# Kernel optimization log

Hardware: AMD Instinct MI355X
Metric: run time of the kernel (lower is better)

## Reference

```python
import math
import jax, jax.numpy as jnp
import numpy as np

L, H, D, T_BLOCK, V = 4, 8, 512, 2048, 32000
B, T = 2, 2048
HD = D // H
EPS = 1e-5


def setup_inputs() -> dict:
    key = jax.random.key(0)
    ks = jax.random.split(key, 8)
    nrm = lambda k, s: (jax.random.normal(k, s, jnp.float32) * 0.02)
    return {
        "wte": nrm(ks[0], (V, D)),
        "wpe": nrm(ks[1], (T_BLOCK, D)),
        "ln1_w": jnp.ones((L, D), jnp.float32),
        "ln1_b": jnp.zeros((L, D), jnp.float32),
        "attn_w": nrm(ks[2], (L, D, 3 * D)),
        "attn_b": jnp.zeros((L, 3 * D), jnp.float32),
        "proj_w": nrm(ks[3], (L, D, D)),
        "proj_b": jnp.zeros((L, D), jnp.float32),
        "ln2_w": jnp.ones((L, D), jnp.float32),
        "ln2_b": jnp.zeros((L, D), jnp.float32),
        "fc_w": nrm(ks[4], (L, D, 4 * D)),
        "fc_b": jnp.zeros((L, 4 * D), jnp.float32),
        "fc2_w": nrm(ks[5], (L, 4 * D, D)),
        "fc2_b": jnp.zeros((L, D), jnp.float32),
        "lnf_w": jnp.ones((D,), jnp.float32),
        "lnf_b": jnp.zeros((D,), jnp.float32),
        "idx": jax.random.randint(ks[6], (B, T), 0, V, dtype=jnp.int32),
    }


def _layer_norm(x, w, b):
    mu = jnp.mean(x, axis=-1, keepdims=True)
    var = jnp.mean(jnp.square(x - mu), axis=-1, keepdims=True)
    return (x - mu) * jax.lax.rsqrt(var + EPS) * w + b


def _gpt_forward(wte, wpe, ln1_w, ln1_b, attn_w, attn_b, proj_w, proj_b,
                 ln2_w, ln2_b, fc_w, fc_b, fc2_w, fc2_b, lnf_w, lnf_b, idx):
    t = idx.shape[1]
    x = wte[idx] + wpe[:t]  # [B,T,D]
    causal = jnp.tril(jnp.ones((t, t), bool))  # [T,T]
    scale = 1.0 / math.sqrt(HD)

    def block(x, p):
        l1w, l1b, aw, ab, pw, pb, l2w, l2b, fw, fb, f2w, f2b = p
        h = _layer_norm(x, l1w, l1b)
        qkv = h @ aw + ab  # [B,T,3D]
        q, k, v = jnp.split(qkv, 3, axis=-1)
        q = q.reshape(B, t, H, HD).transpose(0, 2, 1, 3)  # [B,H,T,hd]
        k = k.reshape(B, t, H, HD).transpose(0, 2, 1, 3)
        v = v.reshape(B, t, H, HD).transpose(0, 2, 1, 3)
        att = jnp.einsum('bhqd,bhkd->bhqk', q, k) * scale
        att = jnp.where(causal, att, -jnp.inf)
        att = jax.nn.softmax(att, axis=-1)
        y = jnp.einsum('bhqk,bhkd->bhqd', att, v)
        y = y.transpose(0, 2, 1, 3).reshape(B, t, D)
        x = x + (y @ pw + pb)
        h2 = _layer_norm(x, l2w, l2b)
        x = x + (jax.nn.gelu(h2 @ fw + fb, approximate=False) @ f2w + f2b)
        return x, None

    x, _ = jax.lax.scan(block, x, (ln1_w, ln1_b, attn_w, attn_b, proj_w, proj_b,
                                   ln2_w, ln2_b, fc_w, fc_b, fc2_w, fc2_b))
    x = _layer_norm(x, lnf_w, lnf_b)
    return x @ wte.T  # tied lm_head: [B,T,V]


def reference(wte, wpe, ln1_w, ln1_b, attn_w, attn_b, proj_w, proj_b,
              ln2_w, ln2_b, fc_w, fc_b, fc2_w, fc2_b, lnf_w, lnf_b, idx):
    return _gpt_forward(wte, wpe, ln1_w, ln1_b, attn_w, attn_b, proj_w, proj_b,
                        ln2_w, ln2_b, fc_w, fc_b, fc2_w, fc2_b, lnf_w, lnf_b, idx)
```

## Files before the change

### kernel.cpp

```cpp
#include <hip/hip_runtime.h>
#include <math.h>

#define Lc 4
#define Hc 8
#define Dc 512
#define Vc 32000
#define Bc 2
#define Tc 2048
#define HDc 64
#define Mc (Bc*Tc)
#define D3c (3*Dc)
#define D4c (4*Dc)

typedef unsigned short u16;
typedef unsigned int u32;
typedef __attribute__((ext_vector_type(8))) short bf16x8;
typedef __attribute__((ext_vector_type(4))) float f32x4;

__device__ __forceinline__ float bf2f(u16 u){ union{u32 i; float f;} v; v.i=((u32)u)<<16; return v.f; }
__device__ __forceinline__ u16 f2bf(float f){ union{float f; u32 i;} v; v.f=f; u32 x=v.i; return (u16)((x + 0x7fffu + ((x>>16)&1u))>>16); }

__device__ __forceinline__ void gld16(const void* g, void* l){
    __builtin_amdgcn_global_load_lds((const __attribute__((address_space(1))) u32*)g,
                                     (__attribute__((address_space(3))) u32*)l, 16, 0, 0);
}

#define CVT_TOTAL 30043136
__device__ __attribute__((aligned(16))) u16  g_cvt[CVT_TOTAL];
__device__ __attribute__((aligned(16))) float g_x[(size_t)Mc*Dc];
__device__ __attribute__((aligned(16))) u16  g_h[(size_t)Mc*Dc];
__device__ u32 g_flag;

__global__ void detect_kernel(const u32* __restrict__ p){
    if(threadIdx.x == 0) g_flag = (p[0] == 0x3F800000u) ? 1u : 0u;
}

__global__ void convert_kernel(const void* __restrict__ src, u16* __restrict__ dst, int n){
    int i = blockIdx.x*256 + threadIdx.x;
    if(i >= n) return;
    if(g_flag) dst[i] = f2bf(((const float*)src)[i]);
    else       dst[i] = ((const u16*)src)[i];
}

__global__ void embed_kernel(const u16* __restrict__ wte, const u16* __restrict__ wpe,
                             const int* __restrict__ idx, float* __restrict__ x){
    int tid = blockIdx.x*256 + threadIdx.x;
    int row = tid >> 6;
    int d8 = (tid & 63) << 3;
    int tok = idx[row];
    int t = row & (Tc-1);
    union{uint4 v; u16 u[8];} a, b;
    a.v = *(const uint4*)(wte + (size_t)tok*Dc + d8);
    b.v = *(const uint4*)(wpe + (size_t)t*Dc + d8);
    float* o = x + (size_t)row*Dc + d8;
    #pragma unroll
    for(int i=0;i<8;i++) o[i] = bf2f(a.u[i]) + bf2f(b.u[i]);
}

__global__ void ln_kernel(const float* __restrict__ x, const u16* __restrict__ w,
                          const u16* __restrict__ b, u16* __restrict__ out){
    int wv = threadIdx.x >> 6, lane = threadIdx.x & 63;
    int row = blockIdx.x*4 + wv;
    const float* xr = x + (size_t)row*Dc + lane*8;
    float f[8];
    *(float4*)(f)   = *(const float4*)xr;
    *(float4*)(f+4) = *(const float4*)(xr+4);
    float s=0.f, s2=0.f;
    #pragma unroll
    for(int i=0;i<8;i++){ s+=f[i]; s2+=f[i]*f[i]; }
    #pragma unroll
    for(int off=32; off; off>>=1){ s += __shfl_xor(s,off,64); s2 += __shfl_xor(s2,off,64); }
    float mean = s*(1.f/Dc);
    float var  = s2*(1.f/Dc) - mean*mean;
    float rstd = rsqrtf(var + 1e-5f);
    union{uint4 v; u16 u[8];} w8, b8;
    w8.v = *(const uint4*)(w + lane*8);
    b8.v = *(const uint4*)(b + lane*8);
    u16 o[8];
    #pragma unroll
    for(int i=0;i<8;i++) o[i] = f2bf((f[i]-mean)*rstd*bf2f(w8.u[i]) + bf2f(b8.u[i]));
    *(uint4*)(out + (size_t)row*Dc + lane*8) = *(uint4*)o;
}

__global__ void transpose_kernel(const u16* __restrict__ src, u16* __restrict__ dst, int K, int N){
    __shared__ u16 tile[32][33];
    int l = blockIdx.z;
    const u16* s = src + (size_t)l*K*N;
    u16* d = dst + (size_t)l*K*N;
    int n0 = blockIdx.x*32, k0 = blockIdx.y*32;
    int tx = threadIdx.x, ty = threadIdx.y;
    #pragma unroll
    for(int i=0;i<4;i++) tile[ty+8*i][tx] = s[(size_t)(k0+ty+8*i)*N + n0+tx];
    __syncthreads();
    #pragma unroll
    for(int i=0;i<4;i++) d[(size_t)(n0+ty+8*i)*K + k0+tx] = tile[tx][ty+8*i];
}

template<bool BIAS, bool RESF, bool GELU, bool OUTDYN>
__global__ __launch_bounds__(256)
void gemm_bt(const u16* __restrict__ A, const u16* __restrict__ Bt,
             const u16* __restrict__ bias, const float* __restrict__ res,
             void* __restrict__ Cv, int N, int K){
    __shared__ bf16x8 As8[128*8];
    __shared__ bf16x8 Bs8[128*8];
    u16* As = (u16*)As8; u16* Bs = (u16*)Bs8;
    int tid = threadIdx.x;
    int wv = __builtin_amdgcn_readfirstlane(tid >> 6);
    int lane = tid & 63;
    int l15 = lane & 15, quad = lane >> 4;
    int m0 = blockIdx.y*128, n0 = blockIdx.x*128;
    int wm = (wv>>1)*64, wn = (wv&1)*64;
    f32x4 acc[4][4] = {};
    const bf16x8* Asv = (const bf16x8*)As;
    const bf16x8* Bsv = (const bf16x8*)Bs;
    int ab = (wm + l15)*8 + quad;
    int bb = (wn + l15)*8 + quad;
    for(int k0=0; k0<K; k0+=64){
        #pragma unroll
        for(int p=0;p<4;p++){
            int c = p*256 + wv*64 + lane;
            int r = c>>3, cc = c&7;
            gld16(A + (size_t)(m0+r)*K + k0 + cc*8, As + (size_t)(p*256+wv*64)*8);
        }
        #pragma unroll
        for(int p=0;p<4;p++){
            int c = p*256 + wv*64 + lane;
            int r = c>>3, cc = c&7;
            gld16(Bt + (size_t)(n0+r)*K + k0 + cc*8, Bs + (size_t)(p*256+wv*64)*8);
        }
        __syncthreads();
        #pragma unroll
        for(int kc=0;kc<2;kc++){
            bf16x8 av[4], bv[4];
            #pragma unroll
            for(int i=0;i<4;i++) av[i] = Asv[ab + i*128 + kc*4];
            #pragma unroll
            for(int i=0;i<4;i++) bv[i] = Bsv[bb + i*128 + kc*4];
            #pragma unroll
            for(int mi=0;mi<4;mi++)
            #pragma unroll
            for(int ni=0;ni<4;ni++)
                acc[mi][ni] = __builtin_amdgcn_mfma_f32_16x16x32_bf16(av[mi], bv[ni], acc[mi][ni], 0, 0, 0);
        }
        __syncthreads();
    }
    u32 f32out = OUTDYN ? g_flag : 0u;
    #pragma unroll
    for(int ni=0;ni<4;ni++){
        int col = n0 + wn + ni*16 + l15;
        float bvv = BIAS ? bf2f(bias[col]) : 0.f;
        #pragma unroll
        for(int mi=0;mi<4;mi++){
            int row = m0 + wm + mi*16 + quad*4;
            #pragma unroll
            for(int r=0;r<4;r++){
                float v = acc[mi][ni][r] + bvv;
                if(GELU) v = 0.5f*v*(1.f + erff(v*0.70710678118654752f));
                size_t off = (size_t)(row + r)*N + col;
                if(RESF){ ((float*)Cv)[off] = v + res[off]; }
                else if(OUTDYN){
                    if(f32out) ((float*)Cv)[off] = v;
                    else       ((u16*)Cv)[off] = f2bf(v);
                }
                else ((u16*)Cv)[off] = f2bf(v);
            }
        }
    }
}

__global__ __launch_bounds__(256)
void attn_kernel(const u16* __restrict__ qkv, u16* __restrict__ y){
    __shared__ bf16x8 qk8[1024];
    __shared__ __align__(16) u16 Vt[64*72];
    __shared__ __align__(16) u16 P[4][16][72];
    u16* Qs = (u16*)qk8;
    u16* Ks = Qs + 64*64;
    int tid = threadIdx.x;
    int wv = __builtin_amdgcn_readfirstlane(tid>>6);
    int lane = tid & 63;
    int l15 = lane & 15, quad = lane >> 4;
    int q0 = blockIdx.x * 64;
    int b = blockIdx.y >> 3, hh = blockIdx.y & 7;
    const u16* base = qkv + (size_t)b*Tc*D3c + hh*HDc;
    const u16* Qg = base;
    const u16* Kg = base + Dc;
    const u16* Vg = base + 2*Dc;
    #pragma unroll
    for(int p=0;p<2;p++){
        int c = p*256 + wv*64 + lane;
        int r = c>>3, sg = c&7;
        gld16(Qg + (size_t)(q0+r)*D3c + sg*8, Qs + (size_t)(p*256+wv*64)*8);
    }
    f32x4 o[4] = {};
    float m_[4], l_[4];
    #pragma unroll
    for(int r=0;r<4;r++){ m_[r] = -INFINITY; l_[r] = 0.f; }
    int nkb = (q0>>6) + 1;
    for(int kb=0; kb<nkb; kb++){
        __syncthreads();
        #pragma unroll
        for(int p=0;p<2;p++){
            int c = p*256 + wv*64 + lane;
            int r = c>>3, sg = c&7;
            gld16(Kg + (size_t)(kb*64+r)*D3c + sg*8, Ks + (size_t)(p*256+wv*64)*8);
        }
        #pragma unroll
        for(int p=0;p<2;p++){
            int s = p*256 + tid;
            int key = s & 63, dsg = s >> 6;
            union{uint4 v; u16 u[8];} tv;
            tv.v = *(const uint4*)(Vg + (size_t)(kb*64+key)*D3c + dsg*8);
            #pragma unroll
            for(int j=0;j<8;j++) Vt[(dsg*8+j)*72 + key] = tv.u[j];
        }
        __syncthreads();
        f32x4 s4[4] = {};
        const bf16x8* Qs8 = (const bf16x8*)Qs;
        const bf16x8* Ks8 = (const bf16x8*)Ks;
        #pragma unroll
        for(int kc=0;kc<2;kc++){
            bf16x8 aq = Qs8[(wv*16+l15)*8 + kc*4 + quad];
            #pragma unroll
            for(int ni=0;ni<4;ni++){
                bf16x8 bk = Ks8[(ni*16+l15)*8 + kc*4 + quad];
                s4[ni] = __builtin_amdgcn_mfma_f32_16x16x32_bf16(aq, bk, s4[ni], 0,0,0);
            }
        }
        int qrow = q0 + wv*16 + quad*4;
        int kcol = kb*64 + l15;
        float pp[4][4];
        #pragma unroll
        for(int r=0;r<4;r++){
            float mx = -INFINITY;
            #pragma unroll
            for(int ni=0;ni<4;ni++){
                float sv = (kcol + ni*16 <= qrow + r) ? s4[ni][r] : -INFINITY;
                pp[ni][r] = sv;
                mx = fmaxf(mx, sv);
            }
            #pragma unroll
            for(int off=1; off<16; off<<=1) mx = fmaxf(mx, __shfl_xor(mx, off, 64));
            float mn = fmaxf(m_[r], mx);
            float al = __expf((m_[r] - mn)*0.125f);
            m_[r] = mn;
            float rs = 0.f;
            #pragma unroll
            for(int ni=0;ni<4;ni++){
                float pv = __expf((pp[ni][r] - mn)*0.125f);
                pp[ni][r] = pv;
                rs += pv;
            }
            #pragma unroll
            for(int off=1; off<16; off<<=1) rs += __shfl_xor(rs, off, 64);
            l_[r] = l_[r]*al + rs;
            #pragma unroll
            for(int di=0;di<4;di++) o[di][r] *= al;
        }
        #pragma unroll
        for(int ni=0;ni<4;ni++)
        #pragma unroll
        for(int r=0;r<4;r++)
            P[wv][quad*4+r][ni*16+l15] = f2bf(pp[ni][r]);
        __syncthreads();
        #pragma unroll
        for(int kc=0;kc<2;kc++){
            bf16x8 ap = *(const bf16x8*)&P[wv][l15][kc*32 + quad*8];
            #pragma unroll
            for(int di=0;di<4;di++){
                bf16x8 bv = *(const bf16x8*)&Vt[(di*16+l15)*72 + kc*32 + quad*8];
                o[di] = __builtin_amdgcn_mfma_f32_16x16x32_bf16(ap, bv, o[di], 0,0,0);
            }
        }
    }
    size_t ob = ((size_t)b*Tc + q0 + wv*16 + quad*4)*Dc + hh*HDc;
    #pragma unroll
    for(int r=0;r<4;r++){
        float inv = 1.f / l_[r];
        #pragma unroll
        for(int di=0;di<4;di++)
            y[ob + (size_t)r*Dc + di*16 + l15] = f2bf(o[di][r]*inv);
    }
}

extern "C" void kernel_launch(void* const* d_in, const int* in_sizes, int n_in,
                              void* d_out, int out_size, void* d_ws, size_t ws_size,
                              hipStream_t stream) {
    (void)in_sizes; (void)n_in; (void)out_size; (void)d_ws; (void)ws_size;
    const int* idx = (const int*)d_in[16];
    u16* out = (u16*)d_out;

    detect_kernel<<<1, 64, 0, stream>>>((const u32*)d_in[2]);

    static const size_t cvt_off[16] = {
        0,          16384000,   17432576, 17434624, 17436672, 20582400,
        20588544,   21637120,   21639168, 21641216, 21643264, 25837568,
        25845760,   30040064,   30042112, 30042624 };
    static const int cvt_n[16] = {
        16384000, 1048576, 2048, 2048, 3145728, 6144,
        1048576,  2048,    2048, 2048, 4194304, 8192,
        4194304,  2048,    512,  512 };
    u16* cvt_base;
    hipGetSymbolAddress((void**)&cvt_base, HIP_SYMBOL(g_cvt));
    float* x;  hipGetSymbolAddress((void**)&x, HIP_SYMBOL(g_x));
    u16* hbuf; hipGetSymbolAddress((void**)&hbuf, HIP_SYMBOL(g_h));
    for(int i=0;i<16;i++)
        convert_kernel<<<(cvt_n[i]+255)/256, 256, 0, stream>>>(d_in[i], cvt_base + cvt_off[i], cvt_n[i]);

    const u16* wte    = cvt_base + cvt_off[0];
    const u16* wpe    = cvt_base + cvt_off[1];
    const u16* ln1w   = cvt_base + cvt_off[2];
    const u16* ln1b   = cvt_base + cvt_off[3];
    const u16* attn_w = cvt_base + cvt_off[4];
    const u16* attn_b = cvt_base + cvt_off[5];
    const u16* proj_w = cvt_base + cvt_off[6];
    const u16* proj_b = cvt_base + cvt_off[7];
    const u16* ln2w   = cvt_base + cvt_off[8];
    const u16* ln2b   = cvt_base + cvt_off[9];
    const u16* fc_w   = cvt_base + cvt_off[10];
    const u16* fc_b   = cvt_base + cvt_off[11];
    const u16* fc2_w  = cvt_base + cvt_off[12];
    const u16* fc2_b  = cvt_base + cvt_off[13];
    const u16* lnf_w  = cvt_base + cvt_off[14];
    const u16* lnf_b  = cvt_base + cvt_off[15];

    u16* qkvb = out;
    u16* yb   = qkvb + (size_t)Mc*D3c;
    u16* ub   = yb   + (size_t)Mc*Dc;
    u16* awT  = ub   + (size_t)Mc*D4c;
    u16* pwT  = awT  + (size_t)Lc*Dc*D3c;
    u16* fwT  = pwT  + (size_t)Lc*Dc*Dc;
    u16* f2wT = fwT  + (size_t)Lc*Dc*D4c;

    dim3 tb(32, 8);
    transpose_kernel<<<dim3(D3c/32, Dc/32, Lc), tb, 0, stream>>>(attn_w, awT, Dc, D3c);
    transpose_kernel<<<dim3(Dc/32,  Dc/32, Lc), tb, 0, stream>>>(proj_w, pwT, Dc, Dc);
    transpose_kernel<<<dim3(D4c/32, Dc/32, Lc), tb, 0, stream>>>(fc_w,  fwT, Dc, D4c);
    transpose_kernel<<<dim3(Dc/32, D4c/32, Lc), tb, 0, stream>>>(fc2_w, f2wT, D4c, Dc);

    embed_kernel<<<Mc/4, 256, 0, stream>>>(wte, wpe, idx, x);

    for (int l = 0; l < Lc; l++) {
        ln_kernel<<<Mc/4, 256, 0, stream>>>(x, ln1w + l*Dc, ln1b + l*Dc, hbuf);
        gemm_bt<true,false,false,false><<<dim3(D3c/128, Mc/128), 256, 0, stream>>>(
            hbuf, awT + (size_t)l*Dc*D3c, attn_b + l*D3c, nullptr, qkvb, D3c, Dc);
        attn_kernel<<<dim3(Tc/64, Bc*Hc), 256, 0, stream>>>(qkvb, yb);
        gemm_bt<true,true,false,false><<<dim3(Dc/128, Mc/128), 256, 0, stream>>>(
            yb, pwT + (size_t)l*Dc*Dc, proj_b + l*Dc, x, x, Dc, Dc);
        ln_kernel<<<Mc/4, 256, 0, stream>>>(x, ln2w + l*Dc, ln2b + l*Dc, hbuf);
        gemm_bt<true,false,true,false><<<dim3(D4c/128, Mc/128), 256, 0, stream>>>(
            hbuf, fwT + (size_t)l*Dc*D4c, fc_b + l*D4c, nullptr, ub, D4c, Dc);
        gemm_bt<true,true,false,false><<<dim3(Dc/128, Mc/128), 256, 0, stream>>>(
            ub, f2wT + (size_t)l*D4c*Dc, fc2_b + l*Dc, x, x, Dc, D4c);
    }
    ln_kernel<<<Mc/4, 256, 0, stream>>>(x, lnf_w, lnf_b, hbuf);
    gemm_bt<false,false,false,true><<<dim3(Vc/128, Mc/128), 256, 0, stream>>>(
        hbuf, wte, nullptr, nullptr, out, Vc, Dc);
}
```

Baseline: 1.741 ms.

## Fuse weight conversions, shrink GEMM M-tile, write V pre-transposed from QKV GEMM

Replaces the sixteen per-tensor convert launches with a single vectorized kernel that picks each source by offset. Templates the GEMM on its M-tile so the narrow-N GEMMs (QKV, proj, fc2) launch with 64-row tiles and more blocks. The QKV GEMM epilogue now writes V directly into a [B,H,HD,T] buffer, so attention can load V with async global-to-LDS copies instead of transposing it by hand in shared memory. This also drops one barrier before the PV MFMAs. The extra buffer sits past the weight transposes in the output scratch region, and the V writes are strided 8-byte stores.

```diff
diff --git a/kernel.cpp b/kernel.cpp
--- a/kernel.cpp
+++ b/kernel.cpp
@@ -14,6 +14,7 @@
 
 typedef unsigned short u16;
 typedef unsigned int u32;
+typedef unsigned long long u64;
 typedef __attribute__((ext_vector_type(8))) short bf16x8;
 typedef __attribute__((ext_vector_type(4))) float f32x4;
 
@@ -35,11 +36,32 @@
     if(threadIdx.x == 0) g_flag = (p[0] == 0x3F800000u) ? 1u : 0u;
 }
 
-__global__ void convert_kernel(const void* __restrict__ src, u16* __restrict__ dst, int n){
-    int i = blockIdx.x*256 + threadIdx.x;
-    if(i >= n) return;
-    if(g_flag) dst[i] = f2bf(((const float*)src)[i]);
-    else       dst[i] = ((const u16*)src)[i];
+struct CvtPtrs { const void* p[16]; };
+
+__global__ void convert_all(CvtPtrs ptrs, u16* __restrict__ dst){
+    int t8 = (blockIdx.x*256 + threadIdx.x) << 3;
+    if(t8 >= CVT_TOTAL) return;
+    #define OFF1 16384000
+    #define SEL(i, off) { bool ge = (t8 >= (off)); base = ge ? (off) : base; src = ge ? ptrs.p[i] : src; }
+    int base = 0;
+    const void* src = ptrs.p[0];
+    SEL(1, 16384000) SEL(2, 17432576) SEL(3, 17434624) SEL(4, 17436672)
+    SEL(5, 20582400) SEL(6, 20588544) SEL(7, 21637120) SEL(8, 21639168)
+    SEL(9, 21641216) SEL(10,21643264) SEL(11,25837568) SEL(12,25845760)
+    SEL(13,30040064) SEL(14,30042112) SEL(15,30042624)
+    #undef SEL
+    int local = t8 - base;
+    if(g_flag){
+        const float* s = (const float*)src + local;
+        float4 f0 = *(const float4*)s;
+        float4 f1 = *(const float4*)(s+4);
+        u16 o[8];
+        o[0]=f2bf(f0.x); o[1]=f2bf(f0.y); o[2]=f2bf(f0.z); o[3]=f2bf(f0.w);
+        o[4]=f2bf(f1.x); o[5]=f2bf(f1.y); o[6]=f2bf(f1.z); o[7]=f2bf(f1.w);
+        *(uint4*)(dst + t8) = *(uint4*)o;
+    } else {
+        *(uint4*)(dst + t8) = *(const uint4*)((const u16*)src + local);
+    }
 }
 
 __global__ void embed_kernel(const u16* __restrict__ wte, const u16* __restrict__ wpe,
@@ -96,48 +118,48 @@
     for(int i=0;i<4;i++) d[(size_t)(n0+ty+8*i)*K + k0+tx] = tile[tx][ty+8*i];
 }
 
-template<bool BIAS, bool RESF, bool GELU, bool OUTDYN>
+template<int BM, bool BIAS, bool RESF, bool GELU, bool OUTDYN, bool VSPLIT>
 __global__ __launch_bounds__(256)
 void gemm_bt(const u16* __restrict__ A, const u16* __restrict__ Bt,
              const u16* __restrict__ bias, const float* __restrict__ res,
-             void* __restrict__ Cv, int N, int K){
-    __shared__ bf16x8 As8[128*8];
+             void* __restrict__ Cv, u16* __restrict__ vt, int N, int K){
+    constexpr int PA = BM/32;
+    constexpr int MI = BM/32;
+    __shared__ bf16x8 As8[BM*8];
     __shared__ bf16x8 Bs8[128*8];
     u16* As = (u16*)As8; u16* Bs = (u16*)Bs8;
     int tid = threadIdx.x;
     int wv = __builtin_amdgcn_readfirstlane(tid >> 6);
     int lane = tid & 63;
     int l15 = lane & 15, quad = lane >> 4;
-    int m0 = blockIdx.y*128, n0 = blockIdx.x*128;
-    int wm = (wv>>1)*64, wn = (wv&1)*64;
-    f32x4 acc[4][4] = {};
+    int m0 = blockIdx.y*BM, n0 = blockIdx.x*128;
+    int wm = (wv>>1)*(BM/2), wn = (wv&1)*64;
+    f32x4 acc[MI][4] = {};
     const bf16x8* Asv = (const bf16x8*)As;
     const bf16x8* Bsv = (const bf16x8*)Bs;
     int ab = (wm + l15)*8 + quad;
     int bb = (wn + l15)*8 + quad;
     for(int k0=0; k0<K; k0+=64){
         #pragma unroll
+        for(int p=0;p<PA;p++){
+            int c = p*256 + wv*64 + lane;
+            gld16(A + (size_t)(m0 + (c>>3))*K + k0 + (c&7)*8, As + (size_t)(p*256+wv*64)*8);
+        }
+        #pragma unroll
         for(int p=0;p<4;p++){
             int c = p*256 + wv*64 + lane;
-            int r = c>>3, cc = c&7;
-            gld16(A + (size_t)(m0+r)*K + k0 + cc*8, As + (size_t)(p*256+wv*64)*8);
-        }
-        #pragma unroll
-        for(int p=0;p<4;p++){
-            int c = p*256 + wv*64 + lane;
-            int r = c>>3, cc = c&7;
-            gld16(Bt + (size_t)(n0+r)*K + k0 + cc*8, Bs + (size_t)(p*256+wv*64)*8);
+            gld16(Bt + (size_t)(n0 + (c>>3))*K + k0 + (c&7)*8, Bs + (size_t)(p*256+wv*64)*8);
         }
         __syncthreads();
         #pragma unroll
         for(int kc=0;kc<2;kc++){
-            bf16x8 av[4], bv[4];
-            #pragma unroll
-            for(int i=0;i<4;i++) av[i] = Asv[ab + i*128 + kc*4];
+            bf16x8 av[MI], bv[4];
+            #pragma unroll
+            for(int i=0;i<MI;i++) av[i] = Asv[ab + i*128 + kc*4];
             #pragma unroll
             for(int i=0;i<4;i++) bv[i] = Bsv[bb + i*128 + kc*4];
             #pragma unroll
-            for(int mi=0;mi<4;mi++)
+            for(int mi=0;mi<MI;mi++)
             #pragma unroll
             for(int ni=0;ni<4;ni++)
                 acc[mi][ni] = __builtin_amdgcn_mfma_f32_16x16x32_bf16(av[mi], bv[ni], acc[mi][ni], 0, 0, 0);
@@ -150,31 +172,41 @@
         int col = n0 + wn + ni*16 + l15;
         float bvv = BIAS ? bf2f(bias[col]) : 0.f;
         #pragma unroll
-        for(int mi=0;mi<4;mi++){
+        for(int mi=0;mi<MI;mi++){
             int row = m0 + wm + mi*16 + quad*4;
-            #pragma unroll
-            for(int r=0;r<4;r++){
-                float v = acc[mi][ni][r] + bvv;
-                if(GELU) v = 0.5f*v*(1.f + erff(v*0.70710678118654752f));
-                size_t off = (size_t)(row + r)*N + col;
-                if(RESF){ ((float*)Cv)[off] = v + res[off]; }
-                else if(OUTDYN){
-                    if(f32out) ((float*)Cv)[off] = v;
-                    else       ((u16*)Cv)[off] = f2bf(v);
+            if(VSPLIT && col >= 2*Dc){
+                int c2 = col - 2*Dc;
+                int hh2 = c2 >> 6, dd = c2 & 63;
+                int bb2 = row >> 11, tt = row & (Tc-1);
+                union{ u64 u; u16 h[4]; } pk;
+                #pragma unroll
+                for(int r=0;r<4;r++) pk.h[r] = f2bf(acc[mi][ni][r] + bvv);
+                *(u64*)(vt + (((size_t)(bb2*Hc + hh2)*HDc + dd) << 11) + tt) = pk.u;
+            } else {
+                #pragma unroll
+                for(int r=0;r<4;r++){
+                    float v = acc[mi][ni][r] + bvv;
+                    if(GELU) v = 0.5f*v*(1.f + erff(v*0.70710678118654752f));
+                    size_t off = (size_t)(row + r)*N + col;
+                    if(RESF){ ((float*)Cv)[off] = v + res[off]; }
+                    else if(OUTDYN){
+                        if(f32out) ((float*)Cv)[off] = v;
+                        else       ((u16*)Cv)[off] = f2bf(v);
+                    }
+                    else ((u16*)Cv)[off] = f2bf(v);
                 }
-                else ((u16*)Cv)[off] = f2bf(v);
             }
         }
     }
 }
 
 __global__ __launch_bounds__(256)
-void attn_kernel(const u16* __restrict__ qkv, u16* __restrict__ y){
-    __shared__ bf16x8 qk8[1024];
-    __shared__ __align__(16) u16 Vt[64*72];
+void attn_kernel(const u16* __restrict__ qkv, const u16* __restrict__ vt, u16* __restrict__ y){
+    __shared__ bf16x8 qkv8[1536];
     __shared__ __align__(16) u16 P[4][16][72];
-    u16* Qs = (u16*)qk8;
+    u16* Qs = (u16*)qkv8;
     u16* Ks = Qs + 64*64;
+    u16* Vs = Ks + 64*64;
     int tid = threadIdx.x;
     int wv = __builtin_amdgcn_readfirstlane(tid>>6);
     int lane = tid & 63;
@@ -184,12 +216,11 @@
     const u16* base = qkv + (size_t)b*Tc*D3c + hh*HDc;
     const u16* Qg = base;
     const u16* Kg = base + Dc;
-    const u16* Vg = base + 2*Dc;
+    const u16* Vg = vt + (size_t)(b*Hc + hh)*HDc*Tc;
     #pragma unroll
     for(int p=0;p<2;p++){
         int c = p*256 + wv*64 + lane;
-        int r = c>>3, sg = c&7;
-        gld16(Qg + (size_t)(q0+r)*D3c + sg*8, Qs + (size_t)(p*256+wv*64)*8);
+        gld16(Qg + (size_t)(q0+(c>>3))*D3c + (c&7)*8, Qs + (size_t)(p*256+wv*64)*8);
     }
     f32x4 o[4] = {};
     float m_[4], l_[4];
@@ -201,17 +232,12 @@
         #pragma unroll
         for(int p=0;p<2;p++){
             int c = p*256 + wv*64 + lane;
-            int r = c>>3, sg = c&7;
-            gld16(Kg + (size_t)(kb*64+r)*D3c + sg*8, Ks + (size_t)(p*256+wv*64)*8);
+            gld16(Kg + (size_t)(kb*64+(c>>3))*D3c + (c&7)*8, Ks + (size_t)(p*256+wv*64)*8);
         }
         #pragma unroll
         for(int p=0;p<2;p++){
-            int s = p*256 + tid;
-            int key = s & 63, dsg = s >> 6;
-            union{uint4 v; u16 u[8];} tv;
-            tv.v = *(const uint4*)(Vg + (size_t)(kb*64+key)*D3c + dsg*8);
-            #pragma unroll
-            for(int j=0;j<8;j++) Vt[(dsg*8+j)*72 + key] = tv.u[j];
+            int c = p*256 + wv*64 + lane;
+            gld16(Vg + (size_t)(c>>3)*Tc + kb*64 + (c&7)*8, Vs + (size_t)(p*256+wv*64)*8);
         }
         __syncthreads();
         f32x4 s4[4] = {};
@@ -261,13 +287,13 @@
         #pragma unroll
         for(int r=0;r<4;r++)
             P[wv][quad*4+r][ni*16+l15] = f2bf(pp[ni][r]);
-        __syncthreads();
+        const bf16x8* Vs8 = (const bf16x8*)Vs;
         #pragma unroll
         for(int kc=0;kc<2;kc++){
             bf16x8 ap = *(const bf16x8*)&P[wv][l15][kc*32 + quad*8];
             #pragma unroll
             for(int di=0;di<4;di++){
-                bf16x8 bv = *(const bf16x8*)&Vt[(di*16+l15)*72 + kc*32 + quad*8];
+                bf16x8 bv = Vs8[(di*16+l15)*8 + kc*4 + quad];
                 o[di] = __builtin_amdgcn_mfma_f32_16x16x32_bf16(ap, bv, o[di], 0,0,0);
             }
         }
@@ -295,16 +321,14 @@
         0,          16384000,   17432576, 17434624, 17436672, 20582400,
         20588544,   21637120,   21639168, 21641216, 21643264, 25837568,
         25845760,   30040064,   30042112, 30042624 };
-    static const int cvt_n[16] = {
-        16384000, 1048576, 2048, 2048, 3145728, 6144,
-        1048576,  2048,    2048, 2048, 4194304, 8192,
-        4194304,  2048,    512,  512 };
     u16* cvt_base;
     hipGetSymbolAddress((void**)&cvt_base, HIP_SYMBOL(g_cvt));
     float* x;  hipGetSymbolAddress((void**)&x, HIP_SYMBOL(g_x));
     u16* hbuf; hipGetSymbolAddress((void**)&hbuf, HIP_SYMBOL(g_h));
-    for(int i=0;i<16;i++)
-        convert_kernel<<<(cvt_n[i]+255)/256, 256, 0, stream>>>(d_in[i], cvt_base + cvt_off[i], cvt_n[i]);
+
+    CvtPtrs cp;
+    for(int i=0;i<16;i++) cp.p[i] = d_in[i];
+    convert_all<<<(CVT_TOTAL/8 + 255)/256, 256, 0, stream>>>(cp, cvt_base);
 
     const u16* wte    = cvt_base + cvt_off[0];
     const u16* wpe    = cvt_base + cvt_off[1];
@@ -330,6 +354,7 @@
     u16* pwT  = awT  + (size_t)Lc*Dc*D3c;
     u16* fwT  = pwT  + (size_t)Lc*Dc*Dc;
     u16* f2wT = fwT  + (size_t)Lc*Dc*D4c;
+    u16* vtb  = f2wT + (size_t)Lc*D4c*Dc;
 
     dim3 tb(32, 8);
     transpose_kernel<<<dim3(D3c/32, Dc/32, Lc), tb, 0, stream>>>(attn_w, awT, Dc, D3c);
@@ -341,18 +366,18 @@
 
     for (int l = 0; l < Lc; l++) {
         ln_kernel<<<Mc/4, 256, 0, stream>>>(x, ln1w + l*Dc, ln1b + l*Dc, hbuf);
-        gemm_bt<true,false,false,false><<<dim3(D3c/128, Mc/128), 256, 0, stream>>>(
-            hbuf, awT + (size_t)l*Dc*D3c, attn_b + l*D3c, nullptr, qkvb, D3c, Dc);
-        attn_kernel<<<dim3(Tc/64, Bc*Hc), 256, 0, stream>>>(qkvb, yb);
-        gemm_bt<true,true,false,false><<<dim3(Dc/128, Mc/128), 256, 0, stream>>>(
-            yb, pwT + (size_t)l*Dc*Dc, proj_b + l*Dc, x, x, Dc, Dc);
+        gemm_bt<64,true,false,false,false,true><<<dim3(D3c/128, Mc/64), 256, 0, stream>>>(
+            hbuf, awT + (size_t)l*Dc*D3c, attn_b + l*D3c, nullptr, qkvb, vtb, D3c, Dc);
+        attn_kernel<<<dim3(Tc/64, Bc*Hc), 256, 0, stream>>>(qkvb, vtb, yb);
+        gemm_bt<64,true,true,false,false,false><<<dim3(Dc/128, Mc/64), 256, 0, stream>>>(
+            yb, pwT + (size_t)l*Dc*Dc, proj_b + l*Dc, x, x, nullptr, Dc, Dc);
         ln_kernel<<<Mc/4, 256, 0, stream>>>(x, ln2w + l*Dc, ln2b + l*Dc, hbuf);
-        gemm_bt<true,false,true,false><<<dim3(D4c/128, Mc/128), 256, 0, stream>>>(
-            hbuf, fwT + (size_t)l*Dc*D4c, fc_b + l*D4c, nullptr, ub, D4c, Dc);
-        gemm_bt<true,true,false,false><<<dim3(Dc/128, Mc/128), 256, 0, stream>>>(
-            ub, f2wT + (size_t)l*D4c*Dc, fc2_b + l*Dc, x, x, Dc, D4c);
+        gemm_bt<128,true,false,true,false,false><<<dim3(D4c/128, Mc/128), 256, 0, stream>>>(
+            hbuf, fwT + (size_t)l*Dc*D4c, fc_b + l*D4c, nullptr, ub, nullptr, D4c, Dc);
+        gemm_bt<64,true,true,false,false,false><<<dim3(Dc/128, Mc/64), 256, 0, stream>>>(
+            ub, f2wT + (size_t)l*D4c*Dc, fc2_b + l*Dc, x, x, nullptr, Dc, D4c);
     }
     ln_kernel<<<Mc/4, 256, 0, stream>>>(x, lnf_w, lnf_b, hbuf);
-    gemm_bt<false,false,false,true><<<dim3(Vc/128, Mc/128), 256, 0, stream>>>(
-        hbuf, wte, nullptr, nullptr, out, Vc, Dc);
-}
+    gemm_bt<128,false,false,false,true,false><<<dim3(Vc/128, Mc/128), 256, 0, stream>>>(
+        hbuf, wte, nullptr, nullptr, out, nullptr, Vc, Dc);
+}
```

Result: faster. 1.651 ms (-5.2%).
